# Optimization experiments

Hardware: AMD Instinct MI355X
Metric: run time of the kernel (lower is better)

Reference implementation:

```python
import jax, jax.numpy as jnp
import numpy as np

EPS = 1e-5

def _layer_norm(x, gamma, beta):
    mu = jnp.mean(x, axis=-1, keepdims=True)
    var = jnp.mean(jnp.square(x - mu), axis=-1, keepdims=True)
    return (x - mu) * jax.lax.rsqrt(var + EPS) * gamma + beta

def setup_inputs() -> dict:
    key = jax.random.key(0)
    ks = jax.random.split(key, 6)
    B, D, H = 8192, 1024, 1024
    x = jax.random.normal(ks[0], (B, D), dtype=jnp.float32)
    h0 = jax.random.normal(ks[1], (B, H), dtype=jnp.float32)
    c0 = jax.random.normal(ks[2], (B, H), dtype=jnp.float32)
    # learned params (orthogonal init approximated by scaled normal for reference purposes)
    weight_h = jax.random.normal(ks[3], (H, 4 * H), dtype=jnp.float32) / np.sqrt(H)
    weight_x = jax.random.normal(ks[4], (D, 4 * H), dtype=jnp.float32) / np.sqrt(D)
    bias = jnp.zeros((4 * H,), dtype=jnp.float32).at[:H].set(1.0)  # forget-gate bias init to 1
    ln1_g = jnp.ones((4 * H,), jnp.float32); ln1_b = jnp.zeros((4 * H,), jnp.float32)
    ln2_g = jnp.ones((4 * H,), jnp.float32); ln2_b = jnp.zeros((4 * H,), jnp.float32)
    ln3_g = jnp.ones((H,), jnp.float32); ln3_b = jnp.zeros((H,), jnp.float32)
    return {"x": x, "h0": h0, "c0": c0, "weight_h": weight_h, "weight_x": weight_x,
            "bias": bias, "ln1_g": ln1_g, "ln1_b": ln1_b, "ln2_g": ln2_g, "ln2_b": ln2_b,
            "ln3_g": ln3_g, "ln3_b": ln3_b}

def reference(x, h0, c0, weight_h, weight_x, bias, ln1_g, ln1_b, ln2_g, ln2_b, ln3_g, ln3_b):
    # gates: [B, 4H] = LN(h0 @ Wh) + LN(x @ Wx) + bias
    gates = _layer_norm(h0 @ weight_h, ln1_g, ln1_b) + _layer_norm(x @ weight_x, ln2_g, ln2_b) + bias
    H = h0.shape[-1]
    f_g, i_g, o_g, c_g = jnp.split(gates, 4, axis=1)  # forget, in, out, cell
    c1 = jax.nn.sigmoid(f_g) * c0 + jax.nn.sigmoid(i_g) * jnp.tanh(c_g)
    h1 = jax.nn.sigmoid(o_g) * jnp.tanh(_layer_norm(c1, ln3_g, ln3_b))
    return (h1, c1)
```

## Files before the change

kernel.cpp:

```cpp
#include <hip/hip_runtime.h>
#include <cstdint>

#define B_ROWS 8192
#define KDIM 1024
#define N4 4096

typedef __attribute__((ext_vector_type(8))) short short8;
typedef __attribute__((ext_vector_type(4))) float float4v;

__device__ __forceinline__ unsigned short f2bf(float f) {
  union { float f; unsigned int u; } v; v.f = f;
  unsigned int r = v.u + 0x7fffu + ((v.u >> 16) & 1u);
  return (unsigned short)(r >> 16);
}

__device__ __forceinline__ float bf2f(unsigned short s) {
  union { unsigned int u; float f; } v; v.u = ((unsigned int)s) << 16;
  return v.f;
}

__device__ __forceinline__ void async16(const unsigned short* g, unsigned short* l) {
  auto gp = (const __attribute__((address_space(1))) unsigned int*)(uintptr_t)g;
  auto lp = (__attribute__((address_space(3))) unsigned int*)(unsigned int)(uintptr_t)l;
  __builtin_amdgcn_global_load_lds(gp, lp, 16, 0, 0);
}

__device__ __forceinline__ float sigm(float v) { return 1.f / (1.f + expf(-v)); }


__global__ __launch_bounds__(256) void cast_bf16(const float* __restrict__ in0,
                                                 unsigned short* __restrict__ out0,
                                                 const float* __restrict__ in1,
                                                 unsigned short* __restrict__ out1) {
  const float* in = blockIdx.y ? in1 : in0;
  unsigned short* out = blockIdx.y ? out1 : out0;
  int i = (blockIdx.x * 256 + threadIdx.x) * 4;
  float4 v = *(const float4*)(in + i);
  ushort4 o;
  o.x = f2bf(v.x); o.y = f2bf(v.y); o.z = f2bf(v.z); o.w = f2bf(v.w);
  *(ushort4*)(out + i) = o;
}

__global__ __launch_bounds__(256) void transpose_cast(const float* __restrict__ W0,
                                                      unsigned short* __restrict__ Wt0,
                                                      const float* __restrict__ W1,
                                                      unsigned short* __restrict__ Wt1) {
  const float* W = blockIdx.z ? W1 : W0;
  unsigned short* Wt = blockIdx.z ? Wt1 : Wt0;
  __shared__ float tile[32][33];
  int n0 = blockIdx.x * 32;
  int k0 = blockIdx.y * 32;
  int tx = threadIdx.x & 31;
  int ty = threadIdx.x >> 5;
#pragma unroll
  for (int i = 0; i < 32; i += 8)
    tile[ty + i][tx] = W[(size_t)(k0 + ty + i) * N4 + n0 + tx];
  __syncthreads();
#pragma unroll
  for (int i = 0; i < 32; i += 8)
    Wt[(size_t)(n0 + ty + i) * KDIM + k0 + tx] = f2bf(tile[tx][ty + i]);
}


__global__ __launch_bounds__(256) void gemm_bf16(
    const unsigned short* __restrict__ Ah, const unsigned short* __restrict__ Wth,
    unsigned short* __restrict__ Uh,
    const unsigned short* __restrict__ Ax, const unsigned short* __restrict__ Wtx,
    unsigned short* __restrict__ Ux, int row0) {
  const unsigned short* A; const unsigned short* W; unsigned short* U;
  if (blockIdx.z == 0) { A = Ah; W = Wth; U = Uh; } else { A = Ax; W = Wtx; U = Ux; }

  __shared__ unsigned short ldsA[128 * 64];
  __shared__ unsigned short ldsB[128 * 64];

  const int tid = threadIdx.x;
  const int wave = tid >> 6;
  const int lane = tid & 63;
  const int wm = (wave & 1) * 64;
  const int wn = (wave >> 1) * 64;

  const int m0 = row0 + blockIdx.y * 128;
  const int n0 = blockIdx.x * 128;

  const int r8 = lane >> 3;
  const int c8 = lane & 7;
  const int g8 = (c8 - r8) & 7;
  const unsigned short* gA0 = A + (size_t)(m0 + wave * 32 + r8) * KDIM + g8 * 8;
  const unsigned short* gB0 = W + (size_t)(n0 + wave * 32 + r8) * KDIM + g8 * 8;
  unsigned short* lA0 = ldsA + (wave * 32) * 64;
  unsigned short* lB0 = ldsB + (wave * 32) * 64;

  const short8* fA[2][4];
  const short8* fB[2][4];
#pragma unroll
  for (int kh = 0; kh < 2; ++kh)
#pragma unroll
    for (int i = 0; i < 4; ++i) {
      int ma = wm + i * 16 + (lane & 15);
      int qa = kh * 4 + (lane >> 4);
      fA[kh][i] = (const short8*)(ldsA + ma * 64 + (((qa + ma) & 7) * 8));
      int nb = wn + i * 16 + (lane & 15);
      int qb = kh * 4 + (lane >> 4);
      fB[kh][i] = (const short8*)(ldsB + nb * 64 + (((qb + nb) & 7) * 8));
    }

  float4v acc[4][4];
  float4v zero = {0.f, 0.f, 0.f, 0.f};
#pragma unroll
  for (int i = 0; i < 4; ++i)
#pragma unroll
    for (int j = 0; j < 4; ++j) acc[i][j] = zero;

  for (int kt = 0; kt < KDIM; kt += 64) {
#pragma unroll
    for (int j = 0; j < 4; ++j) {
      async16(gA0 + kt + j * 8 * KDIM, lA0 + j * 8 * 64);
      async16(gB0 + kt + j * 8 * KDIM, lB0 + j * 8 * 64);
    }
    __syncthreads();
#pragma unroll
    for (int kh = 0; kh < 2; ++kh) {
      short8 a[4], b[4];
#pragma unroll
      for (int i = 0; i < 4; ++i) { a[i] = *fA[kh][i]; b[i] = *fB[kh][i]; }
#pragma unroll
      for (int mi = 0; mi < 4; ++mi)
#pragma unroll
        for (int ni = 0; ni < 4; ++ni)
          acc[mi][ni] = __builtin_amdgcn_mfma_f32_16x16x32_bf16(a[mi], b[ni], acc[mi][ni], 0, 0, 0);
    }
    __syncthreads();
  }

  const int colc = lane & 15;
  const int rowq = (lane >> 4) * 4;
  unsigned short* Ub = U + (size_t)(blockIdx.y * 128 + wm + rowq) * N4 + n0 + wn + colc;
#pragma unroll
  for (int mi = 0; mi < 4; ++mi)
#pragma unroll
    for (int r = 0; r < 4; ++r) {
      unsigned short* Urow = Ub + (size_t)(mi * 16 + r) * N4;
#pragma unroll
      for (int ni = 0; ni < 4; ++ni) Urow[ni * 16] = f2bf(acc[mi][ni][r]);
    }
}


__global__ __launch_bounds__(256) void fused_ln_lstm(
    const unsigned short* __restrict__ Uh, const unsigned short* __restrict__ Ux,
    const float* __restrict__ c0, const float* __restrict__ bias,
    const float* __restrict__ g1, const float* __restrict__ b1,
    const float* __restrict__ g2, const float* __restrict__ b2,
    const float* __restrict__ g3, const float* __restrict__ b3,
    float* __restrict__ h1o, float* __restrict__ c1o, int row0) {
  const int t = threadIdx.x;
  const int lane = t & 63;
  const int wv = t >> 6;
  const size_t rloc = blockIdx.x;
  const size_t rabs = rloc + (size_t)row0;

  const ushort4* uh = (const ushort4*)(Uh + rloc * N4);
  const ushort4* ux = (const ushort4*)(Ux + rloc * N4);
  float4 cold = ((const float4*)(c0 + rabs * KDIM))[t];

  float4 vh[4], vx[4];
  float sh = 0.f, qh = 0.f, sx = 0.f, qx = 0.f;
#pragma unroll
  for (int k = 0; k < 4; ++k) {
    ushort4 au = uh[k * 256 + t];
    float4 a; a.x = bf2f(au.x); a.y = bf2f(au.y); a.z = bf2f(au.z); a.w = bf2f(au.w);
    vh[k] = a;
    sh += (a.x + a.y) + (a.z + a.w);
    qh += a.x * a.x + a.y * a.y + a.z * a.z + a.w * a.w;
    ushort4 bu = ux[k * 256 + t];
    float4 b; b.x = bf2f(bu.x); b.y = bf2f(bu.y); b.z = bf2f(bu.z); b.w = bf2f(bu.w);
    vx[k] = b;
    sx += (b.x + b.y) + (b.z + b.w);
    qx += b.x * b.x + b.y * b.y + b.z * b.z + b.w * b.w;
  }
  __shared__ float red[4][4];
#pragma unroll
  for (int o = 32; o > 0; o >>= 1) {
    sh += __shfl_down(sh, o); qh += __shfl_down(qh, o);
    sx += __shfl_down(sx, o); qx += __shfl_down(qx, o);
  }
  if (lane == 0) { red[wv][0] = sh; red[wv][1] = qh; red[wv][2] = sx; red[wv][3] = qx; }
  __syncthreads();
  sh = red[0][0] + red[1][0] + red[2][0] + red[3][0];
  qh = red[0][1] + red[1][1] + red[2][1] + red[3][1];
  sx = red[0][2] + red[1][2] + red[2][2] + red[3][2];
  qx = red[0][3] + red[1][3] + red[2][3] + red[3][3];
  const float inv4 = 1.f / 4096.f;
  const float muh = sh * inv4, mux = sx * inv4;
  const float rsh = rsqrtf(qh * inv4 - muh * muh + 1e-5f);
  const float rsx = rsqrtf(qx * inv4 - mux * mux + 1e-5f);

  float4 gate[4];
#pragma unroll
  for (int k = 0; k < 4; ++k) {
    int j = k * 256 + t;
    float4 G1 = ((const float4*)g1)[j], B1 = ((const float4*)b1)[j];
    float4 G2 = ((const float4*)g2)[j], B2 = ((const float4*)b2)[j];
    float4 BB = ((const float4*)bias)[j];
    float4 a = vh[k], b = vx[k], r;
    r.x = (a.x - muh) * rsh * G1.x + B1.x + (b.x - mux) * rsx * G2.x + B2.x + BB.x;
    r.y = (a.y - muh) * rsh * G1.y + B1.y + (b.y - mux) * rsx * G2.y + B2.y + BB.y;
    r.z = (a.z - muh) * rsh * G1.z + B1.z + (b.z - mux) * rsx * G2.z + B2.z + BB.z;
    r.w = (a.w - muh) * rsh * G1.w + B1.w + (b.w - mux) * rsx * G2.w + B2.w + BB.w;
    gate[k] = r;
  }
  float4 fg = gate[0], ig = gate[1], og = gate[2], cg = gate[3];
  float4 c1v;
  c1v.x = sigm(fg.x) * cold.x + sigm(ig.x) * tanhf(cg.x);
  c1v.y = sigm(fg.y) * cold.y + sigm(ig.y) * tanhf(cg.y);
  c1v.z = sigm(fg.z) * cold.z + sigm(ig.z) * tanhf(cg.z);
  c1v.w = sigm(fg.w) * cold.w + sigm(ig.w) * tanhf(cg.w);

  float sc = (c1v.x + c1v.y) + (c1v.z + c1v.w);
  float qc = c1v.x * c1v.x + c1v.y * c1v.y + c1v.z * c1v.z + c1v.w * c1v.w;
#pragma unroll
  for (int o = 32; o > 0; o >>= 1) { sc += __shfl_down(sc, o); qc += __shfl_down(qc, o); }
  __syncthreads();
  if (lane == 0) { red[wv][0] = sc; red[wv][1] = qc; }
  __syncthreads();
  sc = red[0][0] + red[1][0] + red[2][0] + red[3][0];
  qc = red[0][1] + red[1][1] + red[2][1] + red[3][1];
  const float invH = 1.f / 1024.f;
  const float muc = sc * invH;
  const float rsc = rsqrtf(qc * invH - muc * muc + 1e-5f);
  float4 G3 = ((const float4*)g3)[t], B3 = ((const float4*)b3)[t];
  float4 h1v;
  h1v.x = sigm(og.x) * tanhf((c1v.x - muc) * rsc * G3.x + B3.x);
  h1v.y = sigm(og.y) * tanhf((c1v.y - muc) * rsc * G3.y + B3.y);
  h1v.z = sigm(og.z) * tanhf((c1v.z - muc) * rsc * G3.z + B3.z);
  h1v.w = sigm(og.w) * tanhf((c1v.w - muc) * rsc * G3.w + B3.w);

  ((float4*)(h1o + rabs * KDIM))[t] = h1v;
  ((float4*)(c1o + rabs * KDIM))[t] = c1v;
}


extern "C" void kernel_launch(void* const* d_in, const int* in_sizes, int n_in,
                              void* d_out, int out_size, void* d_ws, size_t ws_size,
                              hipStream_t stream) {
  const float* x    = (const float*)d_in[0];
  const float* h0   = (const float*)d_in[1];
  const float* c0   = (const float*)d_in[2];
  const float* Wh   = (const float*)d_in[3];
  const float* Wx   = (const float*)d_in[4];
  const float* bias = (const float*)d_in[5];
  const float* g1   = (const float*)d_in[6];
  const float* b1   = (const float*)d_in[7];
  const float* g2   = (const float*)d_in[8];
  const float* b2   = (const float*)d_in[9];
  const float* g3   = (const float*)d_in[10];
  const float* b3   = (const float*)d_in[11];
  float* h1o = (float*)d_out;
  float* c1o = h1o + (size_t)B_ROWS * KDIM;

  unsigned short* Ah  = (unsigned short*)d_ws;
  unsigned short* Ax  = Ah + (size_t)B_ROWS * KDIM;
  unsigned short* Wth = Ax + (size_t)B_ROWS * KDIM;
  unsigned short* Wtx = Wth + (size_t)N4 * KDIM;
  unsigned short* U = Wtx + (size_t)N4 * KDIM;
  size_t used = ((size_t)B_ROWS * KDIM * 2 + (size_t)N4 * KDIM * 2) * sizeof(unsigned short);
  size_t rem = ws_size > used ? ws_size - used : 0;
  int chunk = (int)(rem / ((size_t)2 * N4 * sizeof(unsigned short)));
  chunk &= ~127;
  if (chunk > B_ROWS) chunk = B_ROWS;
  if (chunk < 128) chunk = 128;

  cast_bf16<<<dim3(B_ROWS * KDIM / 1024, 2), 256, 0, stream>>>(h0, Ah, x, Ax);
  transpose_cast<<<dim3(N4 / 32, KDIM / 32, 2), 256, 0, stream>>>(Wh, Wth, Wx, Wtx);

  for (int r0 = 0; r0 < B_ROWS; r0 += chunk) {
    int rows = chunk;
    if (r0 + rows > B_ROWS) rows = B_ROWS - r0;
    unsigned short* Uh = U;
    unsigned short* Ux = U + (size_t)rows * N4;
    gemm_bf16<<<dim3(N4 / 128, rows / 128, 2), 256, 0, stream>>>(Ah, Wth, Uh, Ax, Wtx, Ux, r0);
    fused_ln_lstm<<<rows, 256, 0, stream>>>(Uh, Ux, c0, bias, g1, b1, g2, b2, g3, b3, h1o, c1o, r0);
  }
}
```

Before: 373.3 us.

## Rewrite GEMM as 256x256 double-buffered pipelined tile with XCD-aware block remap

The bf16 GEMM now uses 256x256 output tiles with 512 threads and double-buffered LDS. It splits each K-step into four quadrant phases that interleave async global-to-LDS prefetch of the next tile with MFMA work. It also remaps workgroup IDs across the 8 XCDs for L2 locality and raises MFMA priority with s_setprio. The aim is to hide load latency and improve reuse, at the cost of more LDS (128KB), more accumulator registers, and coarser chunk granularity.

```diff
diff --git a/kernel.cpp b/kernel.cpp
--- a/kernel.cpp
+++ b/kernel.cpp
@@ -62,7 +62,7 @@
 }
 
 
-__global__ __launch_bounds__(256) void gemm_bf16(
+__global__ __launch_bounds__(512, 2) void gemm_bf16(
     const unsigned short* __restrict__ Ah, const unsigned short* __restrict__ Wth,
     unsigned short* __restrict__ Uh,
     const unsigned short* __restrict__ Ax, const unsigned short* __restrict__ Wtx,
@@ -70,73 +70,153 @@
   const unsigned short* A; const unsigned short* W; unsigned short* U;
   if (blockIdx.z == 0) { A = Ah; W = Wth; U = Uh; } else { A = Ax; W = Wtx; U = Ux; }
 
-  __shared__ unsigned short ldsA[128 * 64];
-  __shared__ unsigned short ldsB[128 * 64];
+  __shared__ unsigned short ldsA[2 * 256 * 64];
+  __shared__ unsigned short ldsB[2 * 256 * 64];
 
   const int tid = threadIdx.x;
   const int wave = tid >> 6;
   const int lane = tid & 63;
-  const int wm = (wave & 1) * 64;
-  const int wn = (wave >> 1) * 64;
-
-  const int m0 = row0 + blockIdx.y * 128;
-  const int n0 = blockIdx.x * 128;
+  const int wm2 = wave >> 2;
+  const int wn4 = wave & 3;
+
+  const int gx = N4 / 256;
+  const int nwg = gx * (int)gridDim.y;
+  const int f = (int)blockIdx.y * gx + (int)blockIdx.x;
+  const int qq = nwg >> 3, rr = nwg & 7;
+  const int xcd = f & 7, idx = f >> 3;
+  const int wg = (xcd < rr) ? (xcd * (qq + 1) + idx)
+                            : (rr * (qq + 1) + (xcd - rr) * qq + idx);
+  const int bx = wg & (gx - 1);
+  const int by = wg / gx;
+
+  const int m0 = row0 + by * 256;
+  const int n0 = bx * 256;
 
   const int r8 = lane >> 3;
   const int c8 = lane & 7;
-  const int g8 = (c8 - r8) & 7;
-  const unsigned short* gA0 = A + (size_t)(m0 + wave * 32 + r8) * KDIM + g8 * 8;
-  const unsigned short* gB0 = W + (size_t)(n0 + wave * 32 + r8) * KDIM + g8 * 8;
-  unsigned short* lA0 = ldsA + (wave * 32) * 64;
-  unsigned short* lB0 = ldsB + (wave * 32) * 64;
-
-  const short8* fA[2][4];
-  const short8* fB[2][4];
-#pragma unroll
-  for (int kh = 0; kh < 2; ++kh)
-#pragma unroll
-    for (int i = 0; i < 4; ++i) {
-      int ma = wm + i * 16 + (lane & 15);
-      int qa = kh * 4 + (lane >> 4);
-      fA[kh][i] = (const short8*)(ldsA + ma * 64 + (((qa + ma) & 7) * 8));
-      int nb = wn + i * 16 + (lane & 15);
-      int qb = kh * 4 + (lane >> 4);
-      fB[kh][i] = (const short8*)(ldsB + nb * 64 + (((qb + nb) & 7) * 8));
-    }
-
-  float4v acc[4][4];
+  const int g8 = ((c8 - r8) & 7) * 8;
+  const int aE = (wave & 3) * 16 + (wave >> 2) * 128;
+  const int aL = aE + 64;
+  const int bE = (wave >> 1) * 64 + (wave & 1) * 16;
+  const int bL = bE + 32;
+
+  const unsigned short* gAe = A + (size_t)(m0 + aE + r8) * KDIM + g8;
+  const unsigned short* gAl = A + (size_t)(m0 + aL + r8) * KDIM + g8;
+  const unsigned short* gBe = W + (size_t)(n0 + bE + r8) * KDIM + g8;
+  const unsigned short* gBl = W + (size_t)(n0 + bL + r8) * KDIM + g8;
+
+  const int lq = lane & 15, lh = lane >> 4;
+  const int offA0 = (wm2 * 128 + lq) * 64 + ((lh + lq) & 7) * 8;
+  const int offA1 = (wm2 * 128 + lq) * 64 + ((4 + lh + lq) & 7) * 8;
+  const int offB0 = (wn4 * 64 + lq) * 64 + ((lh + lq) & 7) * 8;
+  const int offB1 = (wn4 * 64 + lq) * 64 + ((4 + lh + lq) & 7) * 8;
+
+  float4v acc[8][4];
   float4v zero = {0.f, 0.f, 0.f, 0.f};
 #pragma unroll
-  for (int i = 0; i < 4; ++i)
+  for (int i = 0; i < 8; ++i)
 #pragma unroll
     for (int j = 0; j < 4; ++j) acc[i][j] = zero;
 
-  for (int kt = 0; kt < KDIM; kt += 64) {
-#pragma unroll
-    for (int j = 0; j < 4; ++j) {
-      async16(gA0 + kt + j * 8 * KDIM, lA0 + j * 8 * 64);
-      async16(gB0 + kt + j * 8 * KDIM, lB0 + j * 8 * 64);
-    }
-    __syncthreads();
-#pragma unroll
-    for (int kh = 0; kh < 2; ++kh) {
-      short8 a[4], b[4];
-#pragma unroll
-      for (int i = 0; i < 4; ++i) { a[i] = *fA[kh][i]; b[i] = *fB[kh][i]; }
+  async16(gAe, ldsA + aE * 64);
+  async16(gAe + 8 * KDIM, ldsA + (aE + 8) * 64);
+  async16(gBe, ldsB + bE * 64);
+  async16(gBe + 8 * KDIM, ldsB + (bE + 8) * 64);
+  async16(gBl, ldsB + bL * 64);
+  async16(gBl + 8 * KDIM, ldsB + (bL + 8) * 64);
+  async16(gAl, ldsA + aL * 64);
+  async16(gAl + 8 * KDIM, ldsA + (aL + 8) * 64);
+  asm volatile("s_waitcnt vmcnt(4)\n\ts_barrier" ::: "memory");
+
+  short8 aF[4][2], bF[4][2];
+
+#pragma unroll 2
+  for (int t = 0; t < KDIM / 64; ++t) {
+    const unsigned short* sA = ldsA + (t & 1) * 16384;
+    const unsigned short* sB = ldsB + (t & 1) * 16384;
+    unsigned short* dA = (unsigned short*)ldsA + ((t + 1) & 1) * 16384;
+    unsigned short* dB = (unsigned short*)ldsB + ((t + 1) & 1) * 16384;
+    const int k2 = (t + 1) * 64;
+
+#pragma unroll
+    for (int mi = 0; mi < 4; ++mi) {
+      aF[mi][0] = *(const short8*)(sA + offA0 + mi * 1024);
+      aF[mi][1] = *(const short8*)(sA + offA1 + mi * 1024);
+    }
+#pragma unroll
+    for (int ni = 0; ni < 2; ++ni) {
+      bF[ni][0] = *(const short8*)(sB + offB0 + ni * 1024);
+      bF[ni][1] = *(const short8*)(sB + offB1 + ni * 1024);
+    }
+    async16(gAe + k2, dA + aE * 64);
+    async16(gAe + k2 + 8 * KDIM, dA + (aE + 8) * 64);
+    __builtin_amdgcn_s_setprio(1);
+#pragma unroll
+    for (int kk = 0; kk < 2; ++kk)
 #pragma unroll
       for (int mi = 0; mi < 4; ++mi)
 #pragma unroll
-        for (int ni = 0; ni < 4; ++ni)
-          acc[mi][ni] = __builtin_amdgcn_mfma_f32_16x16x32_bf16(a[mi], b[ni], acc[mi][ni], 0, 0, 0);
-    }
-    __syncthreads();
-  }
+        for (int ni = 0; ni < 2; ++ni)
+          acc[mi][ni] = __builtin_amdgcn_mfma_f32_16x16x32_bf16(aF[mi][kk], bF[ni][kk], acc[mi][ni], 0, 0, 0);
+    __builtin_amdgcn_s_setprio(0);
+    asm volatile("s_waitcnt vmcnt(4)\n\ts_barrier" ::: "memory");
+
+#pragma unroll
+    for (int ni = 0; ni < 2; ++ni) {
+      bF[2 + ni][0] = *(const short8*)(sB + offB0 + (2 + ni) * 1024);
+      bF[2 + ni][1] = *(const short8*)(sB + offB1 + (2 + ni) * 1024);
+    }
+    async16(gBe + k2, dB + bE * 64);
+    async16(gBe + k2 + 8 * KDIM, dB + (bE + 8) * 64);
+    __builtin_amdgcn_s_setprio(1);
+#pragma unroll
+    for (int kk = 0; kk < 2; ++kk)
+#pragma unroll
+      for (int mi = 0; mi < 4; ++mi)
+#pragma unroll
+        for (int ni = 0; ni < 2; ++ni)
+          acc[mi][2 + ni] = __builtin_amdgcn_mfma_f32_16x16x32_bf16(aF[mi][kk], bF[2 + ni][kk], acc[mi][2 + ni], 0, 0, 0);
+    __builtin_amdgcn_s_setprio(0);
+    asm volatile("s_waitcnt vmcnt(4)\n\ts_barrier" ::: "memory");
+
+#pragma unroll
+    for (int mi = 0; mi < 4; ++mi) {
+      aF[mi][0] = *(const short8*)(sA + offA0 + (4 + mi) * 1024);
+      aF[mi][1] = *(const short8*)(sA + offA1 + (4 + mi) * 1024);
+    }
+    async16(gBl + k2, dB + bL * 64);
+    async16(gBl + k2 + 8 * KDIM, dB + (bL + 8) * 64);
+    __builtin_amdgcn_s_setprio(1);
+#pragma unroll
+    for (int kk = 0; kk < 2; ++kk)
+#pragma unroll
+      for (int mi = 0; mi < 4; ++mi)
+#pragma unroll
+        for (int ni = 0; ni < 2; ++ni)
+          acc[4 + mi][ni] = __builtin_amdgcn_mfma_f32_16x16x32_bf16(aF[mi][kk], bF[ni][kk], acc[4 + mi][ni], 0, 0, 0);
+    __builtin_amdgcn_s_setprio(0);
+    asm volatile("s_waitcnt vmcnt(4)\n\ts_barrier" ::: "memory");
+
+    async16(gAl + k2, dA + aL * 64);
+    async16(gAl + k2 + 8 * KDIM, dA + (aL + 8) * 64);
+    __builtin_amdgcn_s_setprio(1);
+#pragma unroll
+    for (int kk = 0; kk < 2; ++kk)
+#pragma unroll
+      for (int mi = 0; mi < 4; ++mi)
+#pragma unroll
+        for (int ni = 0; ni < 2; ++ni)
+          acc[4 + mi][2 + ni] = __builtin_amdgcn_mfma_f32_16x16x32_bf16(aF[mi][kk], bF[2 + ni][kk], acc[4 + mi][2 + ni], 0, 0, 0);
+    __builtin_amdgcn_s_setprio(0);
+    asm volatile("s_waitcnt vmcnt(4)\n\ts_barrier" ::: "memory");
+  }
+  asm volatile("s_waitcnt vmcnt(0)" ::: "memory");
 
   const int colc = lane & 15;
   const int rowq = (lane >> 4) * 4;
-  unsigned short* Ub = U + (size_t)(blockIdx.y * 128 + wm + rowq) * N4 + n0 + wn + colc;
-#pragma unroll
-  for (int mi = 0; mi < 4; ++mi)
+  unsigned short* Ub = U + (size_t)(by * 256 + wm2 * 128 + rowq) * N4 + n0 + wn4 * 64 + colc;
+#pragma unroll
+  for (int mi = 0; mi < 8; ++mi)
 #pragma unroll
     for (int r = 0; r < 4; ++r) {
       unsigned short* Urow = Ub + (size_t)(mi * 16 + r) * N4;
@@ -266,9 +346,9 @@
   size_t used = ((size_t)B_ROWS * KDIM * 2 + (size_t)N4 * KDIM * 2) * sizeof(unsigned short);
   size_t rem = ws_size > used ? ws_size - used : 0;
   int chunk = (int)(rem / ((size_t)2 * N4 * sizeof(unsigned short)));
-  chunk &= ~127;
+  chunk &= ~255;
   if (chunk > B_ROWS) chunk = B_ROWS;
-  if (chunk < 128) chunk = 128;
+  if (chunk < 256) chunk = 256;
 
   cast_bf16<<<dim3(B_ROWS * KDIM / 1024, 2), 256, 0, stream>>>(h0, Ah, x, Ax);
   transpose_cast<<<dim3(N4 / 32, KDIM / 32, 2), 256, 0, stream>>>(Wh, Wth, Wx, Wtx);
@@ -278,7 +358,7 @@
     if (r0 + rows > B_ROWS) rows = B_ROWS - r0;
     unsigned short* Uh = U;
     unsigned short* Ux = U + (size_t)rows * N4;
-    gemm_bf16<<<dim3(N4 / 128, rows / 128, 2), 256, 0, stream>>>(Ah, Wth, Uh, Ax, Wtx, Ux, r0);
+    gemm_bf16<<<dim3(N4 / 256, rows / 256, 2), 512, 0, stream>>>(Ah, Wth, Uh, Ax, Wtx, Ux, r0);
     fused_ln_lstm<<<rows, 256, 0, stream>>>(Uh, Ux, c0, bias, g1, b1, g2, b2, g3, b3, h1o, c1o, r0);
   }
 }
```

Result: no change. 372.2 us (-0.3%).
